# Kernel optimization log

Hardware: AMD Instinct MI355X
Metric: run time of the kernel (lower is better)

Reference implementation:

```python
import jax, jax.numpy as jnp
import numpy as np

EMBED_DIM = 300
HIDDEN = 128
N_CLS = 20
N_NODES = 100000
N_EDGES = 1600000
N_GRAPHS = 512
EPSILON = 1e-06


def setup_inputs() -> dict:
    key = jax.random.key(0)
    ks = jax.random.split(key, 10)
    x_fp16 = jax.random.normal(ks[0], (N_NODES, EMBED_DIM), dtype=jnp.float16)
    ei = jax.random.randint(ks[1], (2, N_EDGES), 0, N_NODES, dtype=jnp.int32)
    batch = jnp.sort(jax.random.randint(ks[2], (N_NODES,), 0, N_GRAPHS, dtype=jnp.int32))
    mask = jax.random.randint(ks[3], (N_NODES,), 0, 2, dtype=jnp.int32).astype(jnp.bool_)
    def glorot(k, fan_in, fan_out):
        s = (6.0 / (fan_in + fan_out)) ** 0.5
        return jax.random.uniform(k, (fan_in, fan_out), jnp.float32, -s, s)
    return {
        "x_fp16": x_fp16, "ei": ei, "batch": batch, "mask": mask,
        "W1": glorot(ks[4], EMBED_DIM, HIDDEN), "b1": jnp.zeros((HIDDEN,), jnp.float32),
        "W2": glorot(ks[5], HIDDEN, HIDDEN), "b2": jnp.zeros((HIDDEN,), jnp.float32),
        "Wout": glorot(ks[6], HIDDEN, N_CLS), "bout": jnp.zeros((N_CLS,), jnp.float32),
    }


def gcn_conv(x, W, b, src, dst, n):
    # PyG GCNConv: x' = D^{-1/2} (A + I) D^{-1/2} (x W) + b
    h = x @ W  # [N, out]
    loop = jnp.arange(n, dtype=src.dtype)
    s = jnp.concatenate([src, loop])
    d = jnp.concatenate([dst, loop])
    deg = jax.ops.segment_sum(jnp.ones_like(d, dtype=h.dtype), d, num_segments=n)
    dinv = jax.lax.rsqrt(deg)  # deg >= 1 thanks to self-loops
    norm = dinv[s] * dinv[d]  # [E+N]
    msg = h[s] * norm[:, None]
    return jax.ops.segment_sum(msg, d, num_segments=n) + b


def reference(x_fp16, ei, batch, mask, W1, b1, W2, b2, Wout, bout):
    n = x_fp16.shape[0]
    src, dst = ei[0], ei[1]
    x = x_fp16.astype(jnp.float32)
    x = jax.nn.relu(gcn_conv(x, W1, b1, src, dst, n))
    x = jax.nn.relu(gcn_conv(x, W2, b2, src, dst, n))
    m = mask.astype(jnp.float32)[:, None]  # [N,1]
    ent_sum = jax.ops.segment_sum(x * m, batch, num_segments=N_GRAPHS)  # [G,H]
    ent_cnt = jax.ops.segment_sum(m, batch, num_segments=N_GRAPHS)  # [G,1]
    doc_vec = ent_sum / (ent_cnt + EPSILON)
    # fallback: mean over all nodes when a graph has no masked entities
    node_sum = jax.ops.segment_sum(x, batch, num_segments=N_GRAPHS)
    node_cnt = jax.ops.segment_sum(jnp.ones((n, 1), jnp.float32), batch, num_segments=N_GRAPHS)
    mean_pool = node_sum / jnp.maximum(node_cnt, 1.0)
    zero = ent_cnt < EPSILON  # [G,1]
    doc_vec = jnp.where(zero, mean_pool, doc_vec)
    return jax.nn.log_softmax(doc_vec @ Wout + bout, axis=1)
```

## Files before the change

kernel.cpp:

```cpp
#include <hip/hip_runtime.h>
#include <hip/hip_fp16.h>

#define NN 100000
#define NE 1600000
#define DIM 300
#define HID 128
#define NC 20
#define NG 512
#define NBK 196
#define BCH 4096

typedef _Float16 h8 __attribute__((ext_vector_type(8)));
typedef float f4 __attribute__((ext_vector_type(4)));

union pack16 { float4 v; __half2 h2[4]; };

__device__ __forceinline__ __half tohalf(float v) {
  if (!(v == v)) v = 0.f;
  v = fminf(fmaxf(v, -60000.f), 60000.f);
  return __float2half(v);
}

__device__ __forceinline__ float load_x(const void* xraw, size_t o, int mode) {
  float v;
  if (mode == 2) v = ((const float*)xraw)[o];
  else {
    unsigned short u = ((const unsigned short*)xraw)[o];
    if (mode == 1) { union { unsigned w; float f; } c; c.w = ((unsigned)u) << 16; v = c.f; }
    else { union { unsigned short s; _Float16 h; } c; c.s = u; v = (float)c.h; }
  }
  if (!(v == v)) v = 0.f;
  return fminf(fmaxf(v, -1e4f), 1e4f);
}


__global__ void k_probe_modes(const unsigned short* __restrict__ xu, unsigned* __restrict__ diag) {
  int b = blockIdx.x, t = threadIdx.x;
  int mode = b % 3, chunk = b / 3;
  float m = 0.f;
  if (mode == 0) {
    int base = chunk * 16384;
    for (int j = t; j < 16384; j += 256) {
      union { unsigned short s; _Float16 h; } c; c.s = xu[base + j];
      float v = fabsf((float)c.h);
      if (v == v && v < 65000.f) m = fmaxf(m, v);
    }
  } else if (mode == 1) {
    int base = chunk * 16384;
    for (int j = t; j < 16384; j += 256) {
      union { unsigned w; float f; } c; c.w = ((unsigned)xu[base + j]) << 16;
      float v = fabsf(c.f);
      if (v == v && v < 1e30f) m = fmaxf(m, v);
    }
  } else {
    const float* xf = (const float*)xu;
    int base = chunk * 8192;
    for (int j = t; j < 8192; j += 256) {
      float v = fabsf(xf[base + j]);
      if (v == v && v < 1e30f) m = fmaxf(m, v);
    }
  }
  for (int off = 32; off; off >>= 1) m = fmaxf(m, __shfl_xor(m, off));
  if ((t & 63) == 0) atomicMax(&diag[20 + mode], __float_as_uint(m));
}

__global__ void k_probe_umax(const unsigned* __restrict__ p, unsigned* __restrict__ slot) {
  __shared__ unsigned red[256];
  int t = threadIdx.x; unsigned m = 0;
  for (int j = t; j < 25000; j += 256) m = max(m, p[j]);
  red[t] = m; __syncthreads();
  for (int off = 128; off; off >>= 1) { if (t < off) red[t] = max(red[t], red[t + off]); __syncthreads(); }
  if (t == 0) *slot = red[0];
}

__global__ void k_probe_ei(const int* __restrict__ e32, unsigned* __restrict__ slot) {
  int i = blockIdx.x * blockDim.x + threadIdx.x;
  int stride = gridDim.x * blockDim.x;
  unsigned z = 0;
  for (; i < 50000; i += stride) if (e32[2 * i + 1] == 0) z++;
  atomicAdd(slot, z);
}

__global__ void k_decide(const unsigned* __restrict__ diag, int* __restrict__ flags) {
  float M16 = __uint_as_float(diag[20]);
  float M32 = __uint_as_float(diag[21]);
  float Mf  = __uint_as_float(diag[22]);
  int xmode = 3;
  if      (Mf  > 3.f && Mf  < 8.f) xmode = 2;
  else if (M32 > 3.f && M32 < 8.f) xmode = 1;
  else if (M16 > 3.f && M16 < 8.f) xmode = 0;
  flags[0] = xmode;
  unsigned uA = diag[24], uB = diag[25];
  bool Ab = (uA >= 32u && uA < 1024u), Bb = (uB >= 32u && uB < 1024u);
  int swap = -1;
  if (Ab && !Bb) swap = 0;
  else if (Bb && !Ab) swap = 1;
  int mint = -1;
  if (swap >= 0) {
    unsigned um = (swap == 0) ? uB : uA;
    if (um <= 1u) mint = 1;
    else if (um >= 65536u) mint = 0;
  }
  flags[2] = (swap == 1) ? 1 : 0;
  flags[1] = (mint == 1) ? 1 : 0;
  flags[4] = (swap >= 0 && mint >= 0) ? 1 : 0;
  flags[3] = (diag[26] >= 49990u) ? 1 : 0;
}


__global__ void k_bhist(const int* __restrict__ e32, const int* __restrict__ flags,
                        int* __restrict__ bcnt) {
  __shared__ int hist[NBK];
  int e64 = flags[3];
  int t = threadIdx.x;
  for (int j = t; j < NBK; j += 256) hist[j] = 0;
  __syncthreads();
  int i = blockIdx.x * blockDim.x + t;
  int stride = gridDim.x * blockDim.x;
  for (; i < NE; i += stride) {
    int s = e64 ? e32[2 * i] : e32[i];
    int d = e64 ? e32[2 * NE + 2 * i] : e32[NE + i];
    if ((unsigned)s < (unsigned)NN && (unsigned)d < (unsigned)NN)
      atomicAdd(&hist[d >> 9], 1);
  }
  __syncthreads();
  for (int j = t; j < NBK; j += 256) if (hist[j]) atomicAdd(&bcnt[j], hist[j]);
}

__global__ void k_bscan(const int* __restrict__ bcnt, int* __restrict__ boff,
                        int* __restrict__ bcur) {
  if (blockIdx.x == 0 && threadIdx.x == 0) {
    int run = 0;
    for (int j = 0; j < NBK; j++) { boff[j] = run; bcur[j] = run; run += bcnt[j]; }
    boff[NBK] = run;
  }
}

__global__ __launch_bounds__(256)
void k_bscatter(const int* __restrict__ e32, const int* __restrict__ flags,
                int* __restrict__ bcur, unsigned* __restrict__ ebuf) {
  __shared__ uint2 stage[BCH];
  __shared__ int hist[NBK];
  __shared__ int lbase[NBK];
  __shared__ int lcur[NBK];
  int e64 = flags[3];
  int t = threadIdx.x;
  for (int j = t; j < NBK; j += 256) { hist[j] = 0; lcur[j] = 0; }
  __syncthreads();
  int start = blockIdx.x * BCH;
  int n = NE - start; if (n > BCH) n = BCH;
  for (int i = t; i < n; i += 256) {
    int idx = start + i;
    int s = e64 ? e32[2 * idx] : e32[idx];
    int d = e64 ? e32[2 * NE + 2 * idx] : e32[NE + idx];
    bool ok = ((unsigned)s < (unsigned)NN) && ((unsigned)d < (unsigned)NN);
    stage[i] = make_uint2(ok ? (unsigned)s : 0xFFFFFFFFu, (unsigned)(ok ? d : 0));
    if (ok) atomicAdd(&hist[d >> 9], 1);
  }
  __syncthreads();
  for (int j = t; j < NBK; j += 256) if (hist[j] > 0) lbase[j] = atomicAdd(&bcur[j], hist[j]);
  __syncthreads();
  for (int i = t; i < n; i += 256) {
    unsigned s = stage[i].x;
    if (s == 0xFFFFFFFFu) continue;
    int d = (int)stage[i].y;
    int b = d >> 9;
    int o = atomicAdd(&lcur[b], 1);
    ebuf[lbase[b] + o] = (s << 9) | (unsigned)(d & 511);
  }
}

__global__ __launch_bounds__(256)
void k_bfinal(const unsigned* __restrict__ ebuf, const int* __restrict__ boff,
              int* __restrict__ row_off, float* __restrict__ dinv, int* __restrict__ csr) {
  __shared__ int ldeg[512];
  __shared__ int lcur[512];
  int b = blockIdx.x, t = threadIdx.x;
  int base = b * 512;
  int nn = NN - base; if (nn > 512) nn = 512;
  for (int j = t; j < 512; j += 256) ldeg[j] = 0;
  __syncthreads();
  int s0 = boff[b], s1 = boff[b + 1];
  for (int e = s0 + t; e < s1; e += 256) atomicAdd(&ldeg[ebuf[e] & 511], 1);
  __syncthreads();
  if (t == 0) {
    int run = s0;
    for (int i = 0; i < nn; i++) { lcur[i] = run; row_off[base + i] = run; run += ldeg[i]; }
    if (b == gridDim.x - 1) row_off[NN] = run;
  }
  __syncthreads();
  for (int j = t; j < nn; j += 256) dinv[base + j] = rsqrtf((float)ldeg[j] + 1.0f);
  for (int e = s0 + t; e < s1; e += 256) {
    unsigned v = ebuf[e];
    int p = atomicAdd(&lcur[v & 511], 1);
    csr[p] = (int)(v >> 9);
  }
}


__global__ void k_gstart(const int* __restrict__ A, const int* __restrict__ B,
                         const int* __restrict__ flags, int* __restrict__ gstart) {
  const int* batch = flags[2] ? B : A;
  int g = blockIdx.x * blockDim.x + threadIdx.x;
  if (g > NG) return;
  if (g == NG) { gstart[NG] = NN; return; }
  int lo = 0, hi = NN;
  while (lo < hi) { int mid = (lo + hi) >> 1; if (batch[mid] < g) lo = mid + 1; else hi = mid; }
  gstart[g] = lo;
}


__global__ void k_prep(const float* __restrict__ W1, const float* __restrict__ W2,
                       _Float16* __restrict__ w1f, _Float16* __restrict__ w2f) {
  int idx = blockIdx.x * blockDim.x + threadIdx.x;
  const int S1 = 10 * 8 * 64 * 8;
  const int S2 = 4 * 8 * 64 * 8;
  if (idx < S1) {
    int j = idx & 7, l = (idx >> 3) & 63, nt = (idx >> 9) & 7, kc = idx >> 12;
    int k = kc * 32 + ((l >> 4) << 3) + j;
    int n = nt * 16 + (l & 15);
    w1f[idx] = (k < DIM) ? (_Float16)W1[k * HID + n] : (_Float16)0.f;
  } else if (idx < S1 + S2) {
    int q = idx - S1;
    int j = q & 7, l = (q >> 3) & 63, nt = (q >> 9) & 7, kc = q >> 12;
    int k = kc * 32 + ((l >> 4) << 3) + j;
    int n = nt * 16 + (l & 15);
    w2f[q] = (_Float16)W2[k * HID + n];
  }
}


__global__ __launch_bounds__(256)
void k_gemm1_mfma(const void* __restrict__ Ain, const _Float16* __restrict__ bfrag,
                  const float* __restrict__ dinv, const int* __restrict__ flags,
                  __half* __restrict__ outg) {
  __shared__ _Float16 xs[64 * 296];
  const int mode = flags[0] & 3;
  int tid = threadIdx.x;
  int w = tid >> 6, l = tid & 63;
  int rowbase = blockIdx.x * 64;
  int rloc = w * 16 + (l & 15);
  int row = rowbase + rloc;
  int k0base = (l >> 4) << 3;

  h8 vtail = {};
  {
    int k0 = 288 + k0base;
    if (row < NN) {
      #pragma unroll
      for (int j = 0; j < 8; j++) {
        int k = k0 + j;
        vtail[j] = (k < DIM) ? (_Float16)load_x(Ain, (size_t)row * DIM + k, mode) : (_Float16)0.f;
      }
    }
  }

  if (mode == 2) {
    const float* xf = (const float*)Ain;
    for (int c = tid; c < 64 * 72; c += 256) {
      int rl = c / 72, k = (c - rl * 72) * 4;
      int r = rowbase + rl;
      _Float16 o0 = 0, o1 = 0, o2 = 0, o3 = 0;
      if (r < NN) {
        float4 fv = *(const float4*)(xf + (size_t)r * DIM + k);
        o0 = (_Float16)fv.x; o1 = (_Float16)fv.y; o2 = (_Float16)fv.z; o3 = (_Float16)fv.w;
      }
      _Float16* p = &xs[rl * 296 + k];
      p[0] = o0; p[1] = o1; p[2] = o2; p[3] = o3;
    }
  } else {
    const unsigned short* xu = (const unsigned short*)Ain;
    for (int c = tid; c < 64 * 72; c += 256) {
      int rl = c / 72, k = (c - rl * 72) * 4;
      int r = rowbase + rl;
      _Float16 o0 = 0, o1 = 0, o2 = 0, o3 = 0;
      if (r < NN) {
        uint2 u = *(const uint2*)(xu + (size_t)r * DIM + k);
        unsigned short s0 = u.x & 0xFFFF, s1 = u.x >> 16, s2 = u.y & 0xFFFF, s3 = u.y >> 16;
        if (mode == 1) {
          union { unsigned w_; float f; } c0, c1, c2, c3;
          c0.w_ = ((unsigned)s0) << 16; c1.w_ = ((unsigned)s1) << 16;
          c2.w_ = ((unsigned)s2) << 16; c3.w_ = ((unsigned)s3) << 16;
          o0 = (_Float16)c0.f; o1 = (_Float16)c1.f; o2 = (_Float16)c2.f; o3 = (_Float16)c3.f;
        } else {
          union { unsigned short s; _Float16 h; } d0, d1, d2, d3;
          d0.s = s0; d1.s = s1; d2.s = s2; d3.s = s3;
          o0 = d0.h; o1 = d1.h; o2 = d2.h; o3 = d3.h;
        }
      }
      _Float16* p = &xs[rl * 296 + k];
      p[0] = o0; p[1] = o1; p[2] = o2; p[3] = o3;
    }
  }
  __syncthreads();

  f4 acc[8];
  f4 zero = {0.f, 0.f, 0.f, 0.f};
  #pragma unroll
  for (int nt = 0; nt < 8; nt++) acc[nt] = zero;

  #pragma unroll
  for (int kc = 0; kc < 9; kc++) {
    h8 a = *(const h8*)&xs[rloc * 296 + kc * 32 + k0base];
    #pragma unroll
    for (int nt = 0; nt < 8; nt++) {
      h8 bv = *(const h8*)&bfrag[(((kc << 3) + nt) * 64 + l) * 8];
      acc[nt] = __builtin_amdgcn_mfma_f32_16x16x32_f16(a, bv, acc[nt], 0, 0, 0);
    }
  }
  #pragma unroll
  for (int nt = 0; nt < 8; nt++) {
    h8 bv = *(const h8*)&bfrag[(((9 << 3) + nt) * 64 + l) * 8];
    acc[nt] = __builtin_amdgcn_mfma_f32_16x16x32_f16(vtail, bv, acc[nt], 0, 0, 0);
  }

  int rb = rowbase + w * 16 + ((l >> 4) << 2);
  int cb = l & 15;
  #pragma unroll
  for (int i = 0; i < 4; i++) {
    int r = rb + i;
    if (r >= NN) continue;
    float dv = dinv[r];
    __half* orow = outg + (size_t)r * HID;
    #pragma unroll
    for (int nt = 0; nt < 8; nt++)
      orow[nt * 16 + cb] = tohalf(acc[nt][i] * dv);
  }
}


__global__ __launch_bounds__(256)
void k_gemm2_mfma(const __half* __restrict__ Ain, const _Float16* __restrict__ bfrag,
                  const float* __restrict__ dinv, __half* __restrict__ outg) {
  __shared__ _Float16 xs[64 * 136];
  int tid = threadIdx.x;
  int w = tid >> 6, l = tid & 63;
  int rowbase = blockIdx.x * 64;
  int rloc = w * 16 + (l & 15);
  int k0base = (l >> 4) << 3;

  for (int c = tid; c < 64 * 16; c += 256) {
    int rl = c >> 4, k = (c & 15) * 8;
    int r = rowbase + rl;
    h8 v = {};
    if (r < NN) v = *(const h8*)((const _Float16*)Ain + (size_t)r * HID + k);
    *(h8*)&xs[rl * 136 + k] = v;
  }
  __syncthreads();

  f4 acc[8];
  f4 zero = {0.f, 0.f, 0.f, 0.f};
  #pragma unroll
  for (int nt = 0; nt < 8; nt++) acc[nt] = zero;

  #pragma unroll
  for (int kc = 0; kc < 4; kc++) {
    h8 a = *(const h8*)&xs[rloc * 136 + kc * 32 + k0base];
    #pragma unroll
    for (int nt = 0; nt < 8; nt++) {
      h8 bv = *(const h8*)&bfrag[(((kc << 3) + nt) * 64 + l) * 8];
      acc[nt] = __builtin_amdgcn_mfma_f32_16x16x32_f16(a, bv, acc[nt], 0, 0, 0);
    }
  }

  int rb = rowbase + w * 16 + ((l >> 4) << 2);
  int cb = l & 15;
  #pragma unroll
  for (int i = 0; i < 4; i++) {
    int r = rb + i;
    if (r >= NN) continue;
    float dv = dinv[r];
    __half* orow = outg + (size_t)r * HID;
    #pragma unroll
    for (int nt = 0; nt < 8; nt++)
      orow[nt * 16 + cb] = tohalf(acc[nt][i] * dv);
  }
}


__global__ __launch_bounds__(256)
void k_agg(const __half* __restrict__ g, const float* __restrict__ dinv,
           const int* __restrict__ row_off, const int* __restrict__ csr,
           const float* __restrict__ bias, __half* __restrict__ out) {
  int tid = threadIdx.x;
  int node = blockIdx.x * 4 + (tid >> 6);
  int l = tid & 63;
  if (node >= NN) return;
  int grp = l >> 4;
  int cl  = l & 15;
  size_t coff = (size_t)cl * 8;

  float a0 = 0.f, a1 = 0.f, a2 = 0.f, a3 = 0.f, a4 = 0.f, a5 = 0.f, a6 = 0.f, a7 = 0.f;
  pack16 r;

  #define ACCUM() do { \
    float2 f0 = __half22float2(r.h2[0]); \
    float2 f1 = __half22float2(r.h2[1]); \
    float2 f2 = __half22float2(r.h2[2]); \
    float2 f3 = __half22float2(r.h2[3]); \
    a0 += f0.x; a1 += f0.y; a2 += f1.x; a3 += f1.y; \
    a4 += f2.x; a5 += f2.y; a6 += f3.x; a7 += f3.y; } while (0)

  int e0 = row_off[node], e1 = row_off[node + 1];
  int e = e0 + grp;
  for (; e + 4 < e1; e += 8) {
    int s1 = csr[e], s2 = csr[e + 4];
    pack16 rA, rB;
    rA.v = *(const float4*)(g + (size_t)s1 * HID + coff);
    rB.v = *(const float4*)(g + (size_t)s2 * HID + coff);
    r = rA; ACCUM();
    r = rB; ACCUM();
  }
  if (e < e1) {
    int s1 = csr[e];
    r.v = *(const float4*)(g + (size_t)s1 * HID + coff);
    ACCUM();
  }
  if (grp == 0) {
    r.v = *(const float4*)(g + (size_t)node * HID + coff);
    ACCUM();
  }
  #undef ACCUM

  a0 += __shfl_xor(a0, 16); a1 += __shfl_xor(a1, 16); a2 += __shfl_xor(a2, 16); a3 += __shfl_xor(a3, 16);
  a4 += __shfl_xor(a4, 16); a5 += __shfl_xor(a5, 16); a6 += __shfl_xor(a6, 16); a7 += __shfl_xor(a7, 16);
  a0 += __shfl_xor(a0, 32); a1 += __shfl_xor(a1, 32); a2 += __shfl_xor(a2, 32); a3 += __shfl_xor(a3, 32);
  a4 += __shfl_xor(a4, 32); a5 += __shfl_xor(a5, 32); a6 += __shfl_xor(a6, 32); a7 += __shfl_xor(a7, 32);

  if (grp == 0) {
    float di = dinv[node];
    const float* bp = bias + coff;
    pack16 w;
    w.h2[0] = __floats2half2_rn(fmaxf(a0 * di + bp[0], 0.f), fmaxf(a1 * di + bp[1], 0.f));
    w.h2[1] = __floats2half2_rn(fmaxf(a2 * di + bp[2], 0.f), fmaxf(a3 * di + bp[3], 0.f));
    w.h2[2] = __floats2half2_rn(fmaxf(a4 * di + bp[4], 0.f), fmaxf(a5 * di + bp[5], 0.f));
    w.h2[3] = __floats2half2_rn(fmaxf(a6 * di + bp[6], 0.f), fmaxf(a7 * di + bp[7], 0.f));
    *(float4*)(out + (size_t)node * HID + coff) = w.v;
  }
}


__global__ __launch_bounds__(256)
void k_pool(const __half* __restrict__ o2, const void* __restrict__ Araw, const void* __restrict__ Braw,
            const int* __restrict__ gstart, const int* __restrict__ flags,
            float* __restrict__ doc) {
  __shared__ float lex[4][HID];
  __shared__ float lnx[4][HID];
  __shared__ int lec[4];
  int gid = blockIdx.x, tid = threadIdx.x;
  int wv = tid >> 6, l = tid & 63;
  int grp = l >> 4, cl = l & 15;
  size_t coff = (size_t)cl * 8;
  const int mint = flags[1];
  const void* mraw = flags[2] ? Araw : Braw;
  const unsigned char* m8 = (const unsigned char*)mraw;
  const int* m32 = (const int*)mraw;
  int s = gstart[gid], e = gstart[gid + 1];

  float ex[8], nx[8];
  #pragma unroll
  for (int j = 0; j < 8; j++) { ex[j] = 0.f; nx[j] = 0.f; }
  int ec = 0;

  for (int n = s + wv * 4 + grp; n < e; n += 16) {
    pack16 r;
    r.v = *(const float4*)(o2 + (size_t)n * HID + coff);
    float2 f0 = __half22float2(r.h2[0]);
    float2 f1 = __half22float2(r.h2[1]);
    float2 f2 = __half22float2(r.h2[2]);
    float2 f3 = __half22float2(r.h2[3]);
    float t0 = f0.x, t1 = f0.y, t2 = f1.x, t3 = f1.y;
    float t4 = f2.x, t5 = f2.y, t6 = f3.x, t7 = f3.y;
    nx[0] += t0; nx[1] += t1; nx[2] += t2; nx[3] += t3;
    nx[4] += t4; nx[5] += t5; nx[6] += t6; nx[7] += t7;
    bool mv = mint ? (m32[n] != 0) : (m8[n] != 0);
    if (mv) {
      ex[0] += t0; ex[1] += t1; ex[2] += t2; ex[3] += t3;
      ex[4] += t4; ex[5] += t5; ex[6] += t6; ex[7] += t7;
      ec++;
    }
  }
  #pragma unroll
  for (int j = 0; j < 8; j++) {
    ex[j] += __shfl_xor(ex[j], 16); ex[j] += __shfl_xor(ex[j], 32);
    nx[j] += __shfl_xor(nx[j], 16); nx[j] += __shfl_xor(nx[j], 32);
  }
  ec += __shfl_xor(ec, 16); ec += __shfl_xor(ec, 32);

  if (grp == 0) {
    #pragma unroll
    for (int j = 0; j < 8; j++) { lex[wv][cl * 8 + j] = ex[j]; lnx[wv][cl * 8 + j] = nx[j]; }
    if (cl == 0) lec[wv] = ec;
  }
  __syncthreads();
  if (tid < HID) {
    float exT = lex[0][tid] + lex[1][tid] + lex[2][tid] + lex[3][tid];
    float nxT = lnx[0][tid] + lnx[1][tid] + lnx[2][tid] + lnx[3][tid];
    int ecT = lec[0] + lec[1] + lec[2] + lec[3];
    int cnt = e - s;
    float dv;
    if (ecT > 0) dv = exT / ((float)ecT + 1e-6f);
    else dv = (cnt > 0) ? nxT / (float)cnt : 0.f;
    doc[gid * HID + tid] = dv;
  }
}

__global__ __launch_bounds__(64)
void k_out(const float* __restrict__ doc, const float* __restrict__ Wout,
           const float* __restrict__ bout, float* __restrict__ out) {
  __shared__ float dv[HID];
  int gid = blockIdx.x, l = threadIdx.x;
  dv[l] = doc[gid * HID + l];
  dv[l + 64] = doc[gid * HID + l + 64];
  __syncthreads();
  float logit = -1e30f;
  if (l < NC) {
    float acc = bout[l];
    for (int k = 0; k < HID; k++) acc += dv[k] * Wout[k * NC + l];
    logit = acc;
  }
  float m = logit;
  for (int off = 32; off; off >>= 1) m = fmaxf(m, __shfl_xor(m, off));
  float ex = (l < NC) ? expf(logit - m) : 0.f;
  float ssum = ex;
  for (int off = 32; off; off >>= 1) ssum += __shfl_xor(ssum, off);
  if (l < NC) out[gid * NC + l] = (logit - m) - logf(ssum);
}

__global__ void k_fail(float* __restrict__ out, float enc) {
  int i = blockIdx.x * blockDim.x + threadIdx.x;
  if (i < NG * NC) out[i] = -enc;
}


extern "C" void kernel_launch(void* const* d_in, const int* in_sizes, int n_in,
                              void* d_out, int out_size, void* d_ws, size_t ws_size,
                              hipStream_t stream) {
  int ix = -1, iei = -1, iA = -1, iB = -1, iW1 = -1, ib1 = -1, iW2 = -1, ib2 = -1, iWo = -1, ibo = -1;
  for (int i = 0; i < n_in; i++) {
    int s = in_sizes[i];
    if (s == 30000000) ix = i;
    else if (s == 3200000) iei = i;
    else if (s == 100000) { if (iA < 0) iA = i; else iB = i; }
    else if (s == 38400) iW1 = i;
    else if (s == 16384) iW2 = i;
    else if (s == 2560) iWo = i;
    else if (s == 20) ibo = i;
    else if (s == 128) { if (ib1 < 0) ib1 = i; else ib2 = i; }
  }
  float* out = (float*)d_out;
  int miss = -1;
  if (ix < 0) miss = 0; else if (iei < 0) miss = 1; else if (iA < 0 || iB < 0) miss = 2;
  else if (iW1 < 0) miss = 3; else if (ib1 < 0 || ib2 < 0) miss = 4; else if (iW2 < 0) miss = 5;
  else if (iWo < 0) miss = 6; else if (ibo < 0) miss = 7;
  if (miss >= 0) {
    k_fail<<<(NG * NC + 255) / 256, 256, 0, stream>>>(out, 8192.f + 64.f * (float)miss);
    return;
  }
  const void* x = d_in[ix];
  const int* e32 = (const int*)d_in[iei];
  const void* Araw = d_in[iA];
  const void* Braw = d_in[iB];
  const float* W1 = (const float*)d_in[iW1];
  const float* b1 = (const float*)d_in[ib1];
  const float* W2 = (const float*)d_in[iW2];
  const float* b2 = (const float*)d_in[ib2];
  const float* Wout = (const float*)d_in[iWo];
  const float* bout = (const float*)d_in[ibo];

  char* ws = (char*)d_ws;
  size_t off = 0;
  auto alloc = [&](size_t bytes) -> char* {
    char* p = ws + off; off += (bytes + 255) & ~(size_t)255; return p;
  };
  float* dinv   = (float*)alloc((size_t)NN * 4);
  int* row_off  = (int*)alloc((size_t)(NN + 1) * 4);
  int* csr      = (int*)alloc((size_t)NE * 4);
  int* bcnt     = (int*)alloc((size_t)NBK * 4);
  int* boff     = (int*)alloc((size_t)(NBK + 1) * 4);
  int* bcur     = (int*)alloc((size_t)NBK * 4);
  int* gstart   = (int*)alloc((size_t)(NG + 1) * 4);
  int* flags    = (int*)alloc(8 * 4);
  _Float16* w1f = (_Float16*)alloc(40960 * 2);
  _Float16* w2f = (_Float16*)alloc(16384 * 2);
  __half* gbuf  = (__half*)alloc((size_t)NN * HID * 2);
  __half* obuf  = (__half*)alloc((size_t)NN * HID * 2);
  float* doc    = (float*)alloc((size_t)NG * HID * 4);
  unsigned* diag = (unsigned*)alloc(64 * 4);
  unsigned* ebuf = (unsigned*)gbuf;

  hipMemsetAsync(bcnt, 0, (size_t)NBK * 4, stream);
  hipMemsetAsync(diag, 0, 64 * 4, stream);

  k_probe_modes<<<96, 256, 0, stream>>>((const unsigned short*)x, diag);
  k_probe_umax<<<1, 256, 0, stream>>>((const unsigned*)Araw, &diag[24]);
  k_probe_umax<<<1, 256, 0, stream>>>((const unsigned*)Braw, &diag[25]);
  k_probe_ei<<<64, 256, 0, stream>>>(e32, &diag[26]);
  k_decide<<<1, 1, 0, stream>>>(diag, flags);

  k_prep<<<(57344 + 255) / 256, 256, 0, stream>>>(W1, W2, w1f, w2f);
  k_bhist<<<1024, 256, 0, stream>>>(e32, flags, bcnt);
  k_bscan<<<1, 64, 0, stream>>>(bcnt, boff, bcur);
  k_bscatter<<<(NE + BCH - 1) / BCH, 256, 0, stream>>>(e32, flags, bcur, ebuf);
  k_bfinal<<<NBK, 256, 0, stream>>>(ebuf, boff, row_off, dinv, csr);
  k_gstart<<<(NG + 1 + 63) / 64, 64, 0, stream>>>((const int*)Araw, (const int*)Braw, flags, gstart);

  k_gemm1_mfma<<<(NN + 63) / 64, 256, 0, stream>>>(x, w1f, dinv, flags, gbuf);
  k_agg<<<NN / 4, 256, 0, stream>>>(gbuf, dinv, row_off, csr, b1, obuf);
  k_gemm2_mfma<<<(NN + 63) / 64, 256, 0, stream>>>(obuf, w2f, dinv, gbuf);
  k_agg<<<NN / 4, 256, 0, stream>>>(gbuf, dinv, row_off, csr, b2, obuf);

  k_pool<<<NG, 256, 0, stream>>>(obuf, Araw, Braw, gstart, flags, doc);
  k_out<<<NG, 64, 0, stream>>>(doc, Wout, bout, out);
}
```

Measured before the change: 361.7 us.

## Split GEMM output columns across waves and stage full K-tail in LDS

Both MFMA GEMM kernels now assign each wave two 16-column output tiles across all 64 rows, instead of 16 rows across all 128 columns. Each wave therefore loads only its own B fragments from global memory, cutting per-wave B traffic fourfold, but it reads four A fragments from LDS per k-step. In gemm1 the scalar per-element load of the last 12 input columns is replaced by staging all 300 columns into a wider, zero-padded LDS row. This removes an uncoalesced tail load but adds LDS footprint and possible bank conflicts from the new stride.

```diff
diff --git a/kernel.cpp b/kernel.cpp
--- a/kernel.cpp
+++ b/kernel.cpp
@@ -230,48 +230,41 @@
 }
 
 
+#define XST 328
+
 __global__ __launch_bounds__(256)
 void k_gemm1_mfma(const void* __restrict__ Ain, const _Float16* __restrict__ bfrag,
                   const float* __restrict__ dinv, const int* __restrict__ flags,
                   __half* __restrict__ outg) {
-  __shared__ _Float16 xs[64 * 296];
+  __shared__ _Float16 xs[64 * XST];
   const int mode = flags[0] & 3;
   int tid = threadIdx.x;
   int w = tid >> 6, l = tid & 63;
   int rowbase = blockIdx.x * 64;
-  int rloc = w * 16 + (l & 15);
-  int row = rowbase + rloc;
   int k0base = (l >> 4) << 3;
-
-  h8 vtail = {};
-  {
-    int k0 = 288 + k0base;
-    if (row < NN) {
-      #pragma unroll
-      for (int j = 0; j < 8; j++) {
-        int k = k0 + j;
-        vtail[j] = (k < DIM) ? (_Float16)load_x(Ain, (size_t)row * DIM + k, mode) : (_Float16)0.f;
-      }
-    }
-  }
-
+  int cb = l & 15;
+
+  for (int t = tid; t < 640; t += 256) {
+    int rl = t / 10, j = t - rl * 10;
+    *(unsigned*)&xs[rl * XST + 300 + j * 2] = 0u;
+  }
   if (mode == 2) {
     const float* xf = (const float*)Ain;
-    for (int c = tid; c < 64 * 72; c += 256) {
-      int rl = c / 72, k = (c - rl * 72) * 4;
+    for (int c = tid; c < 64 * 75; c += 256) {
+      int rl = c / 75, k = (c - rl * 75) * 4;
       int r = rowbase + rl;
       _Float16 o0 = 0, o1 = 0, o2 = 0, o3 = 0;
       if (r < NN) {
         float4 fv = *(const float4*)(xf + (size_t)r * DIM + k);
         o0 = (_Float16)fv.x; o1 = (_Float16)fv.y; o2 = (_Float16)fv.z; o3 = (_Float16)fv.w;
       }
-      _Float16* p = &xs[rl * 296 + k];
+      _Float16* p = &xs[rl * XST + k];
       p[0] = o0; p[1] = o1; p[2] = o2; p[3] = o3;
     }
   } else {
     const unsigned short* xu = (const unsigned short*)Ain;
-    for (int c = tid; c < 64 * 72; c += 256) {
-      int rl = c / 72, k = (c - rl * 72) * 4;
+    for (int c = tid; c < 64 * 75; c += 256) {
+      int rl = c / 75, k = (c - rl * 75) * 4;
       int r = rowbase + rl;
       _Float16 o0 = 0, o1 = 0, o2 = 0, o3 = 0;
       if (r < NN) {
@@ -288,43 +281,47 @@
           o0 = d0.h; o1 = d1.h; o2 = d2.h; o3 = d3.h;
         }
       }
-      _Float16* p = &xs[rl * 296 + k];
+      _Float16* p = &xs[rl * XST + k];
       p[0] = o0; p[1] = o1; p[2] = o2; p[3] = o3;
     }
   }
   __syncthreads();
 
-  f4 acc[8];
+  f4 acc[4][2];
   f4 zero = {0.f, 0.f, 0.f, 0.f};
   #pragma unroll
-  for (int nt = 0; nt < 8; nt++) acc[nt] = zero;
-
-  #pragma unroll
-  for (int kc = 0; kc < 9; kc++) {
-    h8 a = *(const h8*)&xs[rloc * 296 + kc * 32 + k0base];
+  for (int rg = 0; rg < 4; rg++) { acc[rg][0] = zero; acc[rg][1] = zero; }
+
+  #pragma unroll
+  for (int kc = 0; kc < 10; kc++) {
+    int ko = kc * 32 + k0base;
+    h8 a0 = *(const h8*)&xs[(0 * 16 + cb) * XST + ko];
+    h8 a1 = *(const h8*)&xs[(1 * 16 + cb) * XST + ko];
+    h8 a2 = *(const h8*)&xs[(2 * 16 + cb) * XST + ko];
+    h8 a3 = *(const h8*)&xs[(3 * 16 + cb) * XST + ko];
     #pragma unroll
-    for (int nt = 0; nt < 8; nt++) {
+    for (int ntl = 0; ntl < 2; ntl++) {
+      int nt = w * 2 + ntl;
       h8 bv = *(const h8*)&bfrag[(((kc << 3) + nt) * 64 + l) * 8];
-      acc[nt] = __builtin_amdgcn_mfma_f32_16x16x32_f16(a, bv, acc[nt], 0, 0, 0);
-    }
-  }
-  #pragma unroll
-  for (int nt = 0; nt < 8; nt++) {
-    h8 bv = *(const h8*)&bfrag[(((9 << 3) + nt) * 64 + l) * 8];
-    acc[nt] = __builtin_amdgcn_mfma_f32_16x16x32_f16(vtail, bv, acc[nt], 0, 0, 0);
-  }
-
-  int rb = rowbase + w * 16 + ((l >> 4) << 2);
-  int cb = l & 15;
-  #pragma unroll
-  for (int i = 0; i < 4; i++) {
-    int r = rb + i;
-    if (r >= NN) continue;
-    float dv = dinv[r];
-    __half* orow = outg + (size_t)r * HID;
+      acc[0][ntl] = __builtin_amdgcn_mfma_f32_16x16x32_f16(a0, bv, acc[0][ntl], 0, 0, 0);
+      acc[1][ntl] = __builtin_amdgcn_mfma_f32_16x16x32_f16(a1, bv, acc[1][ntl], 0, 0, 0);
+      acc[2][ntl] = __builtin_amdgcn_mfma_f32_16x16x32_f16(a2, bv, acc[2][ntl], 0, 0, 0);
+      acc[3][ntl] = __builtin_amdgcn_mfma_f32_16x16x32_f16(a3, bv, acc[3][ntl], 0, 0, 0);
+    }
+  }
+
+  int rquad = (l >> 4) << 2;
+  #pragma unroll
+  for (int rg = 0; rg < 4; rg++) {
     #pragma unroll
-    for (int nt = 0; nt < 8; nt++)
-      orow[nt * 16 + cb] = tohalf(acc[nt][i] * dv);
+    for (int i = 0; i < 4; i++) {
+      int r = rowbase + rg * 16 + rquad + i;
+      if (r >= NN) continue;
+      float dv = dinv[r];
+      __half* orow = outg + (size_t)r * HID;
+      orow[(w * 2 + 0) * 16 + cb] = tohalf(acc[rg][0][i] * dv);
+      orow[(w * 2 + 1) * 16 + cb] = tohalf(acc[rg][1][i] * dv);
+    }
   }
 }
 
@@ -336,8 +333,8 @@
   int tid = threadIdx.x;
   int w = tid >> 6, l = tid & 63;
   int rowbase = blockIdx.x * 64;
-  int rloc = w * 16 + (l & 15);
   int k0base = (l >> 4) << 3;
+  int cb = l & 15;
 
   for (int c = tid; c < 64 * 16; c += 256) {
     int rl = c >> 4, k = (c & 15) * 8;
@@ -348,32 +345,41 @@
   }
   __syncthreads();
 
-  f4 acc[8];
+  f4 acc[4][2];
   f4 zero = {0.f, 0.f, 0.f, 0.f};
   #pragma unroll
-  for (int nt = 0; nt < 8; nt++) acc[nt] = zero;
+  for (int rg = 0; rg < 4; rg++) { acc[rg][0] = zero; acc[rg][1] = zero; }
 
   #pragma unroll
   for (int kc = 0; kc < 4; kc++) {
-    h8 a = *(const h8*)&xs[rloc * 136 + kc * 32 + k0base];
+    int ko = kc * 32 + k0base;
+    h8 a0 = *(const h8*)&xs[(0 * 16 + cb) * 136 + ko];
+    h8 a1 = *(const h8*)&xs[(1 * 16 + cb) * 136 + ko];
+    h8 a2 = *(const h8*)&xs[(2 * 16 + cb) * 136 + ko];
+    h8 a3 = *(const h8*)&xs[(3 * 16 + cb) * 136 + ko];
     #pragma unroll
-    for (int nt = 0; nt < 8; nt++) {
+    for (int ntl = 0; ntl < 2; ntl++) {
+      int nt = w * 2 + ntl;
       h8 bv = *(const h8*)&bfrag[(((kc << 3) + nt) * 64 + l) * 8];
-      acc[nt] = __builtin_amdgcn_mfma_f32_16x16x32_f16(a, bv, acc[nt], 0, 0, 0);
-    }
-  }
-
-  int rb = rowbase + w * 16 + ((l >> 4) << 2);
-  int cb = l & 15;
-  #pragma unroll
-  for (int i = 0; i < 4; i++) {
-    int r = rb + i;
-    if (r >= NN) continue;
-    float dv = dinv[r];
-    __half* orow = outg + (size_t)r * HID;
+      acc[0][ntl] = __builtin_amdgcn_mfma_f32_16x16x32_f16(a0, bv, acc[0][ntl], 0, 0, 0);
+      acc[1][ntl] = __builtin_amdgcn_mfma_f32_16x16x32_f16(a1, bv, acc[1][ntl], 0, 0, 0);
+      acc[2][ntl] = __builtin_amdgcn_mfma_f32_16x16x32_f16(a2, bv, acc[2][ntl], 0, 0, 0);
+      acc[3][ntl] = __builtin_amdgcn_mfma_f32_16x16x32_f16(a3, bv, acc[3][ntl], 0, 0, 0);
+    }
+  }
+
+  int rquad = (l >> 4) << 2;
+  #pragma unroll
+  for (int rg = 0; rg < 4; rg++) {
     #pragma unroll
-    for (int nt = 0; nt < 8; nt++)
-      orow[nt * 16 + cb] = tohalf(acc[nt][i] * dv);
+    for (int i = 0; i < 4; i++) {
+      int r = rowbase + rg * 16 + rquad + i;
+      if (r >= NN) continue;
+      float dv = dinv[r];
+      __half* orow = outg + (size_t)r * HID;
+      orow[(w * 2 + 0) * 16 + cb] = tohalf(acc[rg][0][i] * dv);
+      orow[(w * 2 + 1) * 16 + cb] = tohalf(acc[rg][1][i] * dv);
+    }
   }
 }
 
```

Measured after the change: 355.3 us. No clear change (-1.8%).
